# Optimization experiments

Measured on AMD Instinct MI355X. Metric: run time of the kernel, lower is better.

## Reference

```python
import jax, jax.numpy as jnp
import numpy as np

D_LATENTS = 256
B, N = 8, 4096
EPS = 1e-5  # BatchNorm eps (torch default)


def _w(k, shape):
    return jax.random.normal(k, shape, jnp.float32) * 0.05


def setup_inputs() -> dict:
    key = jax.random.key(0)
    ks = jax.random.split(key, 20)
    d4, d2, d = D_LATENTS // 4, D_LATENTS // 2, D_LATENTS
    def bn(k):
        k1, k2 = jax.random.split(k)
        g = 1.0 + 0.1 * jax.random.normal(k1, (0,), jnp.float32)  # placeholder
        return g
    inp = {
        "x": jax.random.normal(ks[0], (B, 3, N), jnp.float32),
        "conv1_w": _w(ks[1], (d4, 3)),
        "bn1_g": 1.0 + 0.1 * jax.random.normal(ks[2], (d4,), jnp.float32),
        "bn1_b": 0.1 * jax.random.normal(ks[3], (d4,), jnp.float32),
        "conv2_w": _w(ks[4], (d4, d4)),
        "bn2_g": 1.0 + 0.1 * jax.random.normal(ks[5], (d4,), jnp.float32),
        "bn2_b": 0.1 * jax.random.normal(ks[6], (d4,), jnp.float32),
        "le0_w1": _w(ks[7], (d2, d2)),
        "le0_g1": 1.0 + 0.1 * jax.random.normal(ks[8], (d2,), jnp.float32),
        "le0_b1": 0.1 * jax.random.normal(ks[9], (d2,), jnp.float32),
        "le0_w2": _w(ks[10], (d2, d2)),
        "le0_g2": 1.0 + 0.1 * jax.random.normal(ks[11], (d2,), jnp.float32),
        "le0_b2": 0.1 * jax.random.normal(ks[12], (d2,), jnp.float32),
        "le1_w1": _w(ks[13], (d, d)),
        "le1_g1": 1.0 + 0.1 * jax.random.normal(ks[14], (d,), jnp.float32),
        "le1_b1": 0.1 * jax.random.normal(ks[15], (d,), jnp.float32),
        "le1_w2": _w(ks[16], (d, d)),
        "le1_g2": 1.0 + 0.1 * jax.random.normal(ks[17], (d,), jnp.float32),
        "le1_b2": 0.1 * jax.random.normal(ks[18], (d,), jnp.float32),
    }
    return inp


def _bn_relu(y, g, b, axes, ch_axis):
    # BatchNorm (training-mode batch stats, biased var like torch) + ReLU
    m = jnp.mean(y, axes, keepdims=True)
    v = jnp.var(y, axes, keepdims=True)
    shp = [1] * y.ndim
    shp[ch_axis] = -1
    return jax.nn.relu((y - m) * jax.lax.rsqrt(v + EPS) * g.reshape(shp) + b.reshape(shp))


def _square_distance(src, dst):
    # src [B,S,3], dst [B,N,3] -> [B,S,N]
    return (jnp.sum(src * src, -1, keepdims=True)
            - 2.0 * jnp.einsum('bsc,bnc->bsn', src, dst)
            + jnp.sum(dst * dst, -1)[:, None, :])


def _fps(xyz, npoint):
    # farthest point sampling, deterministic start at index 0
    Bb, Nn, _ = xyz.shape
    def step(carry, _):
        dist_min, farthest = carry
        centroid = jnp.take_along_axis(xyz, farthest[:, None, None], axis=1)  # [B,1,3]
        d = jnp.sum((xyz - centroid) ** 2, -1)  # [B,N]
        dist_min = jnp.minimum(dist_min, d)
        nxt = jnp.argmax(dist_min, -1).astype(jnp.int32)
        return (dist_min, nxt), farthest
    init = (jnp.full((Bb, Nn), 1e10, xyz.dtype), jnp.zeros((Bb,), jnp.int32))
    _, idxs = jax.lax.scan(step, init, None, length=npoint)
    return jnp.transpose(idxs)  # [B, npoint]


def _sample_and_group(npoint, nsample, xyz, points):
    # PCT-style: FPS centers, kNN neighbors (radius unused), concat(rel, center)
    Bb = xyz.shape[0]
    fps_idx = _fps(xyz, npoint)                       # [B,S]
    bidx = jnp.arange(Bb)[:, None]
    new_xyz = xyz[bidx, fps_idx]                      # [B,S,3]
    new_pts = points[bidx, fps_idx]                   # [B,S,D]
    d2 = _square_distance(new_xyz, xyz)               # [B,S,N]
    _, knn_idx = jax.lax.top_k(-d2, nsample)          # [B,S,ns]
    grouped = points[jnp.arange(Bb)[:, None, None], knn_idx]  # [B,S,ns,D]
    center = new_pts[:, :, None, :]
    feat = jnp.concatenate([grouped - center,
                            jnp.broadcast_to(center, grouped.shape)], axis=-1)
    return new_xyz, feat  # [B,S,3], [B,S,ns,2D]


def _local_encoder(x4, w1, g1, b1, w2, g2, b2):
    # x4: [b,n,s,d] -> conv1x1/bn/relu x2 over channel dim, max over s -> [b,out,n]
    y = jnp.einsum('bnsd,od->bnos', x4, w1)
    y = _bn_relu(y, g1, b1, (0, 1, 3), 2)
    y = jnp.einsum('bnis,oi->bnos', y, w2)
    y = _bn_relu(y, g2, b2, (0, 1, 3), 2)
    y = jnp.max(y, axis=3)                # [b,n,out]
    return jnp.transpose(y, (0, 2, 1))    # [b,out,n]


def reference(x, conv1_w, bn1_g, bn1_b, conv2_w, bn2_g, bn2_b,
              le0_w1, le0_g1, le0_b1, le0_w2, le0_g2, le0_b2,
              le1_w1, le1_g1, le1_b1, le1_w2, le1_g2, le1_b2):
    xyz = jnp.transpose(x, (0, 2, 1))                 # [B,N,3]
    y = jnp.einsum('bcn,oc->bon', x, conv1_w)
    y = _bn_relu(y, bn1_g, bn1_b, (0, 2), 1)
    y = jnp.einsum('bcn,oc->bon', y, conv2_w)
    y = _bn_relu(y, bn2_g, bn2_b, (0, 2), 1)
    pts = jnp.transpose(y, (0, 2, 1))                 # [B,N,d4]
    new_xyz, feat = _sample_and_group(512, 32, xyz, pts)       # [B,512,32,d2]
    f0 = _local_encoder(feat, le0_w1, le0_g1, le0_b1, le0_w2, le0_g2, le0_b2)  # [B,d2,512]
    pts1 = jnp.transpose(f0, (0, 2, 1))
    _, feat2 = _sample_and_group(256, 32, new_xyz, pts1)       # [B,256,32,d]
    f1 = _local_encoder(feat2, le1_w1, le1_g1, le1_b1, le1_w2, le1_g2, le1_b2)  # [B,d,256]
    return f1
```

## Files before the change

### kernel.cpp

```cpp
#include <hip/hip_runtime.h>

constexpr int B_  = 8;
constexpr int N_  = 4096;
constexpr int NP1 = 512;
constexpr int NP2 = 256;
constexpr float EPS_ = 1e-5f;

typedef __attribute__((ext_vector_type(8))) short bhalf8;
typedef __attribute__((ext_vector_type(4))) float f32x4;

__device__ inline short f2bf(float f) {
  union { float fv; unsigned u; } v; v.fv = f;
  unsigned r = v.u + 0x7FFFu + ((v.u >> 16) & 1u);
  return (short)(r >> 16);
}

template<int CTRL>
__device__ inline void dpp_amax(unsigned &khi, unsigned &klo) {
  unsigned ohi = (unsigned)__builtin_amdgcn_mov_dpp((int)khi, CTRL, 0xF, 0xF, false);
  unsigned olo = (unsigned)__builtin_amdgcn_mov_dpp((int)klo, CTRL, 0xF, 0xF, false);
  if (ohi > khi || (ohi == khi && olo > klo)) { khi = ohi; klo = olo; }
}
__device__ inline void swz16_amax(unsigned &khi, unsigned &klo) {
  unsigned ohi = (unsigned)__builtin_amdgcn_ds_swizzle((int)khi, 0x401F);
  unsigned olo = (unsigned)__builtin_amdgcn_ds_swizzle((int)klo, 0x401F);
  if (ohi > khi || (ohi == khi && olo > klo)) { khi = ohi; klo = olo; }
}
__device__ inline void x32_amax(unsigned &khi, unsigned &klo) {
  unsigned ohi = (unsigned)__shfl_xor((int)khi, 32);
  unsigned olo = (unsigned)__shfl_xor((int)klo, 32);
  if (ohi > khi || (ohi == khi && olo > klo)) { khi = ohi; klo = olo; }
}
__device__ inline unsigned ford(float f) {
  unsigned u = __float_as_uint(f);
  return u ^ (((unsigned)((int)u >> 31)) | 0x80000000u);
}

constexpr int S_BN1 = 0;
constexpr int S_BN2 = 128;
constexpr int S_L0A = 256;
constexpr int S_L0B = 512;
constexpr int S_L1A = 768;
constexpr int S_L1B = 1280;
constexpr int S_TOTAL = 1792;

constexpr size_t OFF_T1   = 0;
constexpr size_t OFF_YBUF = OFF_T1   + 2097152;
constexpr size_t OFF_PTS1 = OFF_YBUF + 16777216;
constexpr size_t OFF_NXYZ = OFF_PTS1 + 524288;
constexpr size_t OFF_WT2C = OFF_NXYZ + 12288;
constexpr size_t OFF_BW0A = OFF_WT2C + 4096;
constexpr size_t OFF_BW0B = OFF_BW0A + 8192;
constexpr size_t OFF_BW1A = OFF_BW0B + 8192;
constexpr size_t OFF_BW1B = OFF_BW1A + 32768;
constexpr size_t OFF_STAT = OFF_BW1B + 32768;
constexpr size_t OFF_CNT  = OFF_STAT + S_TOTAL;
constexpr size_t OFF_INT  = OFF_CNT + 32;

__device__ inline void prep_elem(int idx, const float* __restrict__ conv2w,
                                 const float* __restrict__ w0a, const float* __restrict__ w0b,
                                 const float* __restrict__ w1a, const float* __restrict__ w1b,
                                 float* __restrict__ wt2c,
                                 short* __restrict__ b0a, short* __restrict__ b0b,
                                 short* __restrict__ b1a, short* __restrict__ b1b) {
  if (idx < 4096) { int d = idx >> 6, o = idx & 63; wt2c[idx] = conv2w[o*64 + d]; return; }
  idx -= 4096;
  const float* w; short* dst; int D;
  if      (idx <  2048) { w = w0a; dst = b0a; D = 128; }
  else if (idx <  4096) { w = w0b; dst = b0b; D = 128; idx -= 2048; }
  else if (idx < 12288) { w = w1a; dst = b1a; D = 256; idx -= 4096; }
  else                  { w = w1b; dst = b1b; D = 256; idx -= 12288; }
  int kblk = idx / D, o = idx % D;
  const float* src = w + (size_t)o*D + kblk*8;
  bhalf8 pk;
#pragma unroll
  for (int j = 0; j < 8; ++j) pk[j] = f2bf(src[j]);
  *(bhalf8*)&dst[(size_t)idx*8] = pk;
}

struct FpsSmem {
  float lx[4096], ly[4096], lz[4096];
  float sx[512], sy[512], sz[512];
  unsigned long long wk[2][8];
  int seli1[512];
  int seli2[256];
};
struct ConvSmem {
  float xs[3][64];
  float redS[4][64], redQ[4][64];
  float sc[64], sh[64];
  float at[64*68];
};

__global__ __launch_bounds__(256) void front_kernel(
    const float* __restrict__ x,
    const float* __restrict__ conv1w, const float* __restrict__ bn1g, const float* __restrict__ bn1b,
    const float* __restrict__ conv2w, const float* __restrict__ bn2g, const float* __restrict__ bn2b,
    const float* __restrict__ w0a, const float* __restrict__ w0b,
    const float* __restrict__ w1a, const float* __restrict__ w1b,
    float* __restrict__ wt2c,
    short* __restrict__ b0a, short* __restrict__ b0b,
    short* __restrict__ b1a, short* __restrict__ b1b,
    float* __restrict__ t1, float* __restrict__ t2,
    float* __restrict__ stats, int* __restrict__ cnt,
    int* __restrict__ sel1, float* __restrict__ nxyz, int* __restrict__ sel2) {
  __shared__ __align__(16) char smem_raw[sizeof(FpsSmem)];
  int t = threadIdx.x;
  if (blockIdx.x < 8) {
    constexpr int NPTS = 4096, NSEL1 = 512, NSEL2 = 256, NT = 256;
    constexpr int K = NPTS / NT, NS = NT / 32;
    FpsSmem& S = *reinterpret_cast<FpsSmem*>(smem_raw);
    int b = blockIdx.x;
    int lane = t & 63, wid = t >> 6;
    const float* cb = x + (size_t)b * 3 * NPTS;
    for (int i = t; i < NPTS; i += NT) {
      S.lx[i] = cb[i]; S.ly[i] = cb[NPTS + i]; S.lz[i] = cb[2*NPTS + i];
    }
    __syncthreads();
    float px[K], py[K], pz[K], dm[K];
#pragma unroll
    for (int k = 0; k < K; ++k) {
      int p = t + k*NT;
      px[k] = S.lx[p]; py[k] = S.ly[p]; pz[k] = S.lz[p];
      dm[k] = 1e10f;
    }
    float cx = S.lx[0], cy = S.ly[0], cz = S.lz[0];
    if (t == 0) { S.seli1[0] = 0; S.sx[0] = cx; S.sy[0] = cy; S.sz[0] = cz; }
    for (int it = 1; it < NSEL1; ++it) {
      float bv = -1.f; int bi = 0;
#pragma unroll
      for (int k = 0; k < K; ++k) {
        float dx = px[k]-cx, dy = py[k]-cy, dz = pz[k]-cz;
        float d = dx*dx + dy*dy + dz*dz;
        float nd = fminf(dm[k], d);
        dm[k] = nd;
        if (nd > bv) { bv = nd; bi = t + k*NT; }
      }
      unsigned khi = __float_as_uint(bv), klo = ~(unsigned)bi;
      dpp_amax<0xB1>(khi, klo);
      dpp_amax<0x4E>(khi, klo);
      dpp_amax<0x141>(khi, klo);
      dpp_amax<0x140>(khi, klo);
      swz16_amax(khi, klo);
      int p = it & 1;
      if ((lane & 31) == 0)
        S.wk[p][wid*2 + (lane >> 5)] = ((unsigned long long)khi << 32) | klo;
      __syncthreads();
      unsigned long long best = S.wk[p][0];
#pragma unroll
      for (int i2 = 1; i2 < NS; ++i2) { unsigned long long v2 = S.wk[p][i2]; if (v2 > best) best = v2; }
      int Bi = (int)(~(unsigned)best);
      cx = S.lx[Bi]; cy = S.ly[Bi]; cz = S.lz[Bi];
      if (t == 0) { S.seli1[it] = Bi; S.sx[it] = cx; S.sy[it] = cy; S.sz[it] = cz; }
    }
    __syncthreads();
    if (t < 64) {
      constexpr int K2 = NSEL1 / 64;
      float qx[K2], qy[K2], qz[K2], dm2[K2];
#pragma unroll
      for (int k = 0; k < K2; ++k) {
        int p = t + k*64;
        qx[k] = S.sx[p]; qy[k] = S.sy[p]; qz[k] = S.sz[p];
        dm2[k] = 1e10f;
      }
      cx = S.sx[0]; cy = S.sy[0]; cz = S.sz[0];
      if (t == 0) S.seli2[0] = 0;
      for (int it = 1; it < NSEL2; ++it) {
        float bv = -1.f; int bi = 0;
#pragma unroll
        for (int k = 0; k < K2; ++k) {
          float dx = qx[k]-cx, dy = qy[k]-cy, dz = qz[k]-cz;
          float d = dx*dx + dy*dy + dz*dz;
          float nd = fminf(dm2[k], d);
          dm2[k] = nd;
          if (nd > bv) { bv = nd; bi = t + k*64; }
        }
        unsigned khi = __float_as_uint(bv), klo = ~(unsigned)bi;
        dpp_amax<0xB1>(khi, klo);
        dpp_amax<0x4E>(khi, klo);
        dpp_amax<0x141>(khi, klo);
        dpp_amax<0x140>(khi, klo);
        swz16_amax(khi, klo);
        x32_amax(khi, klo);
        int Bi = (int)~klo;
        cx = S.sx[Bi]; cy = S.sy[Bi]; cz = S.sz[Bi];
        if (t == 0) S.seli2[it] = Bi;
      }
    } else {
      for (int i = t - 64; i < NSEL1; i += NT - 64) {
        sel1[(size_t)b*NSEL1 + i] = S.seli1[i];
        float* q = nxyz + ((size_t)b*NSEL1 + i)*3;
        q[0] = S.sx[i]; q[1] = S.sy[i]; q[2] = S.sz[i];
      }
    }
    __syncthreads();
    for (int i = t; i < NSEL2; i += NT) sel2[(size_t)b*NSEL2 + i] = S.seli2[i];
    return;
  }
  ConvSmem& C = *reinterpret_cast<ConvSmem*>(smem_raw);
  int cb = blockIdx.x - 8;
  { int idx = cb*256 + t;
    if (idx < 24576) prep_elem(idx, conv2w, w0a, w0b, w1a, w1b, wt2c, b0a, b0b, b1a, b1b); }
  for (int tile = cb; tile < 512; tile += 256) {
    int b = tile >> 6, n0 = (tile & 63) << 6;
    if (t < 192) { int c = t >> 6, nl = t & 63; C.xs[c][nl] = x[((size_t)b*3 + c)*N_ + n0 + nl]; }
    __syncthreads();
    int o = t & 63, ng = t >> 6;
    float w0 = conv1w[o*3+0], w1 = conv1w[o*3+1], w2 = conv1w[o*3+2];
    float ls = 0.f, lq = 0.f;
#pragma unroll
    for (int k = 0; k < 16; ++k) {
      int nl = ng*16 + k;
      float y = C.xs[0][nl]*w0 + C.xs[1][nl]*w1 + C.xs[2][nl]*w2;
      t1[((size_t)b*N_ + n0 + nl)*64 + o] = y;
      ls += y; lq += y*y;
    }
    C.redS[ng][o] = ls; C.redQ[ng][o] = lq;
    __syncthreads();
    if (t < 64) {
      float s = C.redS[0][t]+C.redS[1][t]+C.redS[2][t]+C.redS[3][t];
      float q = C.redQ[0][t]+C.redQ[1][t]+C.redQ[2][t]+C.redQ[3][t];
      atomicAdd(&stats[S_BN1 + t], s);
      atomicAdd(&stats[S_BN1 + 64 + t], q);
    }
    __syncthreads();
  }
  if (t == 0) {
    __threadfence();
    __hip_atomic_fetch_add(&cnt[0], 1, __ATOMIC_ACQ_REL, __HIP_MEMORY_SCOPE_AGENT);
    while (__hip_atomic_load(&cnt[0], __ATOMIC_ACQUIRE, __HIP_MEMORY_SCOPE_AGENT) < 256)
      __builtin_amdgcn_s_sleep(8);
    __threadfence();
  }
  __syncthreads();
  if (t < 64) {
    float m = stats[S_BN1 + t] * (1.f/32768.f);
    float v = stats[S_BN1 + 64 + t] * (1.f/32768.f) - m*m;
    float s = bn1g[t] * rsqrtf(v + EPS_);
    C.sc[t] = s; C.sh[t] = bn1b[t] - m*s;
  }
  __syncthreads();
  for (int tile = cb; tile < 512; tile += 256) {
    int b = tile >> 6, n0 = (tile & 63) << 6;
    constexpr int P = 68;
    for (int e = t; e < 4096; e += 256) {
      int nl = e >> 6, c = e & 63;
      float v = t1[((size_t)b*N_ + n0 + nl)*64 + c];
      C.at[c*P + nl] = fmaxf(v*C.sc[c] + C.sh[c], 0.f);
    }
    __syncthreads();
    int o = t & 63, ng = t >> 6;
    float acc[16];
#pragma unroll
    for (int k = 0; k < 16; ++k) acc[k] = 0.f;
    for (int i = 0; i < 64; ++i) {
      float wv = wt2c[i*64 + o];
      const float* ar = &C.at[i*P + ng*16];
#pragma unroll
      for (int k = 0; k < 16; k += 4) {
        float4 a4 = *(const float4*)(ar + k);
        acc[k+0] += a4.x*wv; acc[k+1] += a4.y*wv;
        acc[k+2] += a4.z*wv; acc[k+3] += a4.w*wv;
      }
    }
    float ls = 0.f, lq = 0.f;
#pragma unroll
    for (int k = 0; k < 16; ++k) {
      float y = acc[k];
      t2[((size_t)b*N_ + n0 + ng*16 + k)*64 + o] = y;
      ls += y; lq += y*y;
    }
    C.redS[ng][o] = ls; C.redQ[ng][o] = lq;
    __syncthreads();
    if (t < 64) {
      float s = C.redS[0][t]+C.redS[1][t]+C.redS[2][t]+C.redS[3][t];
      float q = C.redQ[0][t]+C.redQ[1][t]+C.redQ[2][t]+C.redQ[3][t];
      atomicAdd(&stats[S_BN2 + t], s);
      atomicAdd(&stats[S_BN2 + 64 + t], q);
    }
    __syncthreads();
  }
  if (t == 0) {
    __threadfence();
    __hip_atomic_fetch_add(&cnt[1], 1, __ATOMIC_ACQ_REL, __HIP_MEMORY_SCOPE_AGENT);
    while (__hip_atomic_load(&cnt[1], __ATOMIC_ACQUIRE, __HIP_MEMORY_SCOPE_AGENT) < 256)
      __builtin_amdgcn_s_sleep(8);
    __threadfence();
  }
  __syncthreads();
  {
    int o = t & 63;
    float m = stats[S_BN2 + o] * (1.f/32768.f);
    float v = stats[S_BN2 + 64 + o] * (1.f/32768.f) - m*m;
    float s = bn2g[o] * rsqrtf(v + EPS_);
    float sh = bn2b[o] - m*s;
    for (int tile = cb; tile < 512; tile += 256)
#pragma unroll
      for (int j = 0; j < 16; ++j) {
        size_t idx = (size_t)tile*4096 + j*256 + t;
        t1[idx] = fmaxf(t2[idx]*s + sh, 0.f);
      }
  }
}

template<int NDST, bool XLAY>
__device__ inline void wave_knn(const float* __restrict__ db,
                                float qx, float qy, float qz,
                                int* __restrict__ out32) {
  constexpr int K = NDST / 64;
  int lane = threadIdx.x & 63;
  float q2 = (qx*qx + qy*qy) + qz*qz;
  float d2r[K];
#pragma unroll
  for (int k = 0; k < K; ++k) {
    int j = lane + k*64;
    float xx, yy, zz;
    if (XLAY) { xx = db[j]; yy = db[NDST + j]; zz = db[2*NDST + j]; }
    else      { xx = db[j*3]; yy = db[j*3+1]; zz = db[j*3+2]; }
    float dot = (qx*xx + qy*yy) + qz*zz;
    float p2  = (xx*xx + yy*yy) + zz*zz;
    d2r[k] = (q2 - 2.f*dot) + p2;
  }
  int myout = 0;
  for (int r = 0; r < 32; ++r) {
    float bv = 3e38f; int bi = lane;
#pragma unroll
    for (int k = 0; k < K; ++k) {
      float v = d2r[k];
      if (v < bv) { bv = v; bi = lane + k*64; }
    }
    unsigned khi = ~ford(bv), klo = ~(unsigned)bi;
    dpp_amax<0xB1>(khi, klo);
    dpp_amax<0x4E>(khi, klo);
    dpp_amax<0x141>(khi, klo);
    dpp_amax<0x140>(khi, klo);
    swz16_amax(khi, klo);
    x32_amax(khi, klo);
    int Bi = (int)~klo;
    if (lane == r) myout = Bi;
#pragma unroll
    for (int k = 0; k < K; ++k)
      if (lane + k*64 == Bi) d2r[k] = 3e38f;
  }
  if (lane < 32) out32[lane] = myout;
}

__global__ __launch_bounds__(256) void knn_fused_kernel(
    const float* __restrict__ x, const float* __restrict__ nxyz,
    const int* __restrict__ sel2, int* __restrict__ knn1, int* __restrict__ knn2) {
  int wid = threadIdx.x >> 6;
  int blk = blockIdx.x;
  if (blk < 1024) {
    int q = blk*4 + wid;
    int b = q >> 9, qi = q & 511;
    const float* qp = nxyz + ((size_t)b*NP1 + qi)*3;
    wave_knn<4096, true>(x + (size_t)b*3*N_, qp[0], qp[1], qp[2], knn1 + (size_t)q*32);
  } else {
    int q = (blk - 1024)*4 + wid;
    int b = q >> 8, qi = q & 255;
    int qrow = b*NP1 + sel2[b*NP2 + qi];
    const float* qp = nxyz + (size_t)qrow*3;
    wave_knn<512, false>(nxyz + (size_t)b*NP1*3, qp[0], qp[1], qp[2], knn2 + (size_t)q*32);
  }
}

template<int D, int PW, int NP, int SRCN, int SOFF>
__global__ __launch_bounds__(256) void gemm1_kernel(
    const float* __restrict__ pts, const int* __restrict__ knn,
    const int* __restrict__ cent, const short* __restrict__ bw,
    float* __restrict__ ybuf, float* __restrict__ stats) {
  constexpr int KB = D/8;
  __shared__ __align__(16) short As[64*D];
  __shared__ float cen_s[2*PW];
  __shared__ int kid_s[64];
  __shared__ float sstat[2*D];
  int t = threadIdx.x, blk = blockIdx.x;
  int g0 = blk*2;
  if (t < 64) {
    int grp = t >> 5, s = t & 31;
    kid_s[t] = knn[((size_t)(g0+grp))*32 + s];
  }
  for (int i = t; i < 2*PW; i += 256) {
    int grp = i / PW, d = i % PW;
    int g = g0 + grp; int b = g / NP; int ci = cent[g];
    cen_s[i] = pts[((size_t)b*SRCN + ci)*PW + d];
  }
  for (int i = t; i < 2*D; i += 256) sstat[i] = 0.f;
  __syncthreads();
  for (int task = t; task < 64*KB; task += 256) {
    int row = task / KB, c = task % KB;
    int grp = row >> 5;
    int g = g0 + grp; int b = g / NP;
    int d = c*8;
    float v0,v1,v2,v3,v4,v5,v6,v7;
    if (d < PW) {
      const float* src = pts + ((size_t)b*SRCN + kid_s[row])*PW + d;
      float4 x0 = *(const float4*)src, x1 = *(const float4*)(src+4);
      const float* cc = &cen_s[grp*PW + d];
      v0=x0.x-cc[0]; v1=x0.y-cc[1]; v2=x0.z-cc[2]; v3=x0.w-cc[3];
      v4=x1.x-cc[4]; v5=x1.y-cc[5]; v6=x1.z-cc[6]; v7=x1.w-cc[7];
    } else {
      const float* cc = &cen_s[grp*PW + d - PW];
      v0=cc[0]; v1=cc[1]; v2=cc[2]; v3=cc[3]; v4=cc[4]; v5=cc[5]; v6=cc[6]; v7=cc[7];
    }
    bhalf8 pk;
    pk[0]=f2bf(v0); pk[1]=f2bf(v1); pk[2]=f2bf(v2); pk[3]=f2bf(v3);
    pk[4]=f2bf(v4); pk[5]=f2bf(v5); pk[6]=f2bf(v6); pk[7]=f2bf(v7);
    int a16 = row*KB + (c ^ (row & 7));
    *(bhalf8*)&As[a16*8] = pk;
  }
  __syncthreads();
  int w = t >> 6, l = t & 63, lr = l & 15, lg = l >> 4;
  f32x4 acc[D/16];
#pragma unroll
  for (int ct = 0; ct < D/16; ++ct) acc[ct] = (f32x4){0.f,0.f,0.f,0.f};
  int r = w*16 + lr;
#pragma unroll
  for (int kg = 0; kg < D/32; ++kg) {
    int c = (kg*4 + lg) ^ (r & 7);
    bhalf8 af = *(const bhalf8*)&As[(r*KB + c)*8];
#pragma unroll
    for (int ct = 0; ct < D/16; ++ct) {
      bhalf8 bf = *(const bhalf8*)&bw[((size_t)(kg*4 + lg)*D + ct*16 + lr)*8];
      acc[ct] = __builtin_amdgcn_mfma_f32_16x16x32_bf16(af, bf, acc[ct], 0, 0, 0);
    }
  }
  size_t rb = (size_t)blk*64 + w*16 + lg*4;
#pragma unroll
  for (int ct = 0; ct < D/16; ++ct) {
    int col = ct*16 + lr;
    f32x4 a = acc[ct];
    float* yp = ybuf + rb*D + col;
    yp[0] = a[0]; yp[(size_t)D] = a[1]; yp[(size_t)2*D] = a[2]; yp[(size_t)3*D] = a[3];
    float s = a[0]+a[1]+a[2]+a[3];
    float q = a[0]*a[0]+a[1]*a[1]+a[2]*a[2]+a[3]*a[3];
    s += __shfl_xor(s, 16); q += __shfl_xor(q, 16);
    s += __shfl_xor(s, 32); q += __shfl_xor(q, 32);
    if (lg == 0) { atomicAdd(&sstat[col], s); atomicAdd(&sstat[D+col], q); }
  }
  __syncthreads();
  for (int i = t; i < 2*D; i += 256) atomicAdd(&stats[SOFF+i], sstat[i]);
}

template<int D, int SIN, int SOUT, int CNT>
__global__ __launch_bounds__(256) void gemm2_kernel(
    const float* __restrict__ g1, const float* __restrict__ b1,
    const short* __restrict__ bw, const float* __restrict__ ybuf,
    float* __restrict__ mm, float* __restrict__ stats) {
  __shared__ __align__(16) float scsh[2*D];
  __shared__ float sstat[2*D];
  __shared__ float wmax[4][D], wmin[4][D];
  int t = threadIdx.x, blk = blockIdx.x;
  for (int i = t; i < D; i += 256) {
    float m = stats[SIN + i] * (1.f/(float)CNT);
    float v = stats[SIN + D + i] * (1.f/(float)CNT) - m*m;
    float s = g1[i] * rsqrtf(v + EPS_);
    scsh[i] = s; scsh[D+i] = b1[i] - m*s;
  }
  for (int i = t; i < 2*D; i += 256) sstat[i] = 0.f;
  __syncthreads();
  int w = t >> 6, l = t & 63, lr = l & 15, lg = l >> 4;
  size_t row = (size_t)blk*64 + w*16 + lr;
  const float* yrow = ybuf + row*D;
  f32x4 acc[D/16];
#pragma unroll
  for (int ct = 0; ct < D/16; ++ct) acc[ct] = (f32x4){0.f,0.f,0.f,0.f};
#pragma unroll
  for (int kg = 0; kg < D/32; ++kg) {
    int k = kg*32 + lg*8;
    float4 y0 = *(const float4*)(yrow + k);
    float4 y1 = *(const float4*)(yrow + k + 4);
    bhalf8 af;
    af[0] = f2bf(fmaxf(y0.x*scsh[k+0] + scsh[D+k+0], 0.f));
    af[1] = f2bf(fmaxf(y0.y*scsh[k+1] + scsh[D+k+1], 0.f));
    af[2] = f2bf(fmaxf(y0.z*scsh[k+2] + scsh[D+k+2], 0.f));
    af[3] = f2bf(fmaxf(y0.w*scsh[k+3] + scsh[D+k+3], 0.f));
    af[4] = f2bf(fmaxf(y1.x*scsh[k+4] + scsh[D+k+4], 0.f));
    af[5] = f2bf(fmaxf(y1.y*scsh[k+5] + scsh[D+k+5], 0.f));
    af[6] = f2bf(fmaxf(y1.z*scsh[k+6] + scsh[D+k+6], 0.f));
    af[7] = f2bf(fmaxf(y1.w*scsh[k+7] + scsh[D+k+7], 0.f));
#pragma unroll
    for (int ct = 0; ct < D/16; ++ct) {
      bhalf8 bf = *(const bhalf8*)&bw[((size_t)(kg*4 + lg)*D + ct*16 + lr)*8];
      acc[ct] = __builtin_amdgcn_mfma_f32_16x16x32_bf16(af, bf, acc[ct], 0, 0, 0);
    }
  }
#pragma unroll
  for (int ct = 0; ct < D/16; ++ct) {
    int col = ct*16 + lr;
    f32x4 a = acc[ct];
    float mx = fmaxf(fmaxf(a[0], a[1]), fmaxf(a[2], a[3]));
    float mn = fminf(fminf(a[0], a[1]), fminf(a[2], a[3]));
    mx = fmaxf(mx, __shfl_xor(mx, 16)); mn = fminf(mn, __shfl_xor(mn, 16));
    mx = fmaxf(mx, __shfl_xor(mx, 32)); mn = fminf(mn, __shfl_xor(mn, 32));
    if (lg == 0) { wmax[w][col] = mx; wmin[w][col] = mn; }
    float s = a[0]+a[1]+a[2]+a[3];
    float q = a[0]*a[0]+a[1]*a[1]+a[2]*a[2]+a[3]*a[3];
    s += __shfl_xor(s, 16); q += __shfl_xor(q, 16);
    s += __shfl_xor(s, 32); q += __shfl_xor(q, 32);
    if (lg == 0) { atomicAdd(&sstat[col], s); atomicAdd(&sstat[D+col], q); }
  }
  __syncthreads();
  for (int i = t; i < 2*D; i += 256) {
    int g = i / D, col = i - g*D;
    float mx = fmaxf(wmax[2*g][col], wmax[2*g+1][col]);
    float mn = fminf(wmin[2*g][col], wmin[2*g+1][col]);
    float* mp = mm + ((size_t)blk*2 + g)*2*D;
    mp[col] = mx; mp[D + col] = mn;
    atomicAdd(&stats[SOUT+i], sstat[i]);
  }
}

template<int D, int NP, int SOFF, int CNT, bool TR>
__global__ __launch_bounds__(256) void le3_kernel(
    const float* __restrict__ g2, const float* __restrict__ b2,
    const float* __restrict__ mm, const float* __restrict__ stats,
    float* __restrict__ out) {
  int idx = blockIdx.x*256 + threadIdx.x;
  int g = idx / D, o = idx - g*D;
  float m = stats[SOFF + o] * (1.f/(float)CNT);
  float v = stats[SOFF + D + o] * (1.f/(float)CNT) - m*m;
  float s = g2[o] * rsqrtf(v + EPS_);
  float sh = b2[o] - m*s;
  const float* mp = mm + (size_t)g*2*D;
  float pick = (s >= 0.f) ? mp[o] : mp[D + o];
  float r = fmaxf(pick*s + sh, 0.f);
  if (TR) { int b = g / NP, n = g - b*NP; out[((size_t)b*D + o)*NP + n] = r; }
  else    out[(size_t)g*D + o] = r;
}

extern "C" void kernel_launch(void* const* d_in, const int* in_sizes, int n_in,
                              void* d_out, int out_size, void* d_ws, size_t ws_size,
                              hipStream_t stream) {
  (void)in_sizes; (void)n_in; (void)out_size; (void)ws_size;
  const float* x       = (const float*)d_in[0];
  const float* conv1_w = (const float*)d_in[1];
  const float* bn1_g   = (const float*)d_in[2];
  const float* bn1_b   = (const float*)d_in[3];
  const float* conv2_w = (const float*)d_in[4];
  const float* bn2_g   = (const float*)d_in[5];
  const float* bn2_b   = (const float*)d_in[6];
  const float* le0_w1  = (const float*)d_in[7];
  const float* le0_g1  = (const float*)d_in[8];
  const float* le0_b1  = (const float*)d_in[9];
  const float* le0_w2  = (const float*)d_in[10];
  const float* le0_g2  = (const float*)d_in[11];
  const float* le0_b2  = (const float*)d_in[12];
  const float* le1_w1  = (const float*)d_in[13];
  const float* le1_g1  = (const float*)d_in[14];
  const float* le1_b1  = (const float*)d_in[15];
  const float* le1_w2  = (const float*)d_in[16];
  const float* le1_g2  = (const float*)d_in[17];
  const float* le1_b2  = (const float*)d_in[18];

  float* ws   = (float*)d_ws;
  float* t1   = ws + OFF_T1;
  float* ybuf = ws + OFF_YBUF;
  float* t2   = ybuf;
  float* mm   = t1;
  float* pts1 = ws + OFF_PTS1;
  float* nxyz = ws + OFF_NXYZ;
  float* wt2c = ws + OFF_WT2C;
  short* bw0a = (short*)(ws + OFF_BW0A);
  short* bw0b = (short*)(ws + OFF_BW0B);
  short* bw1a = (short*)(ws + OFF_BW1A);
  short* bw1b = (short*)(ws + OFF_BW1B);
  float* stats = ws + OFF_STAT;
  int*   cnt   = (int*)(ws + OFF_CNT);
  int* fps1 = (int*)(ws + OFF_INT);
  int* fps2 = fps1 + 4096;
  int* knn1 = fps2 + 2048;
  int* knn2 = knn1 + 131072;

  hipMemsetAsync(stats, 0, (S_TOTAL + 32)*sizeof(float), stream);
  front_kernel<<<264, 256, 0, stream>>>(x,
      conv1_w, bn1_g, bn1_b, conv2_w, bn2_g, bn2_b,
      le0_w1, le0_w2, le1_w1, le1_w2,
      wt2c, bw0a, bw0b, bw1a, bw1b,
      t1, t2, stats, cnt, fps1, nxyz, fps2);

  knn_fused_kernel<<<1536, 256, 0, stream>>>(x, nxyz, fps2, knn1, knn2);

  gemm1_kernel<128,  64, 512, 4096, S_L0A><<<2048, 256, 0, stream>>>(t1, knn1, fps1, bw0a, ybuf, stats);
  gemm2_kernel<128, S_L0A, S_L0B, 131072><<<2048, 256, 0, stream>>>(le0_g1, le0_b1, bw0b, ybuf, mm, stats);
  le3_kernel<128, 512, S_L0B, 131072, false><<<2048, 256, 0, stream>>>(le0_g2, le0_b2, mm, stats, pts1);

  gemm1_kernel<256, 128, 256,  512, S_L1A><<<1024, 256, 0, stream>>>(pts1, knn2, fps2, bw1a, ybuf, stats);
  gemm2_kernel<256, S_L1A, S_L1B, 65536><<<1024, 256, 0, stream>>>(le1_g1, le1_b1, bw1b, ybuf, mm, stats);
  le3_kernel<256, 256, S_L1B, 65536, true><<<2048, 256, 0, stream>>>(le1_g2, le1_b2, mm, stats, (float*)d_out);
}
```

Measured before the change: 926.7 us.

## Overlap FPS with kNN and first grouped GEMM via in-kernel flags

The FPS blocks now publish selected centroids in chunks of 64 and raise per-batch/chunk flags. The remaining persistent blocks of the front kernel spin on those flags, run kNN for ready queries, then run the first local-encoder GEMM once all 64 kNN results of a chunk are done, and finally compute the second-level kNN after the sel2 flag. This removes two kernel launches and hides kNN and GEMM1 behind the serial FPS loop. In exchange it relies on co-residency of all 264 blocks for spin-waits, adds sync overhead and atomics, and serializes GEMM1 onto 248 blocks instead of 2048.

Measured after the change: 1.532 ms. 65.3% more time.

```diff
diff --git a/kernel.cpp b/kernel.cpp
--- a/kernel.cpp
+++ b/kernel.cpp
@@ -34,6 +34,26 @@
 __device__ inline unsigned ford(float f) {
   unsigned u = __float_as_uint(f);
   return u ^ (((unsigned)((int)u >> 31)) | 0x80000000u);
+}
+
+__device__ inline void set_flag_after_sync(int* f) {
+  if (threadIdx.x == 0) {
+    __threadfence();
+    __hip_atomic_store(f, 1, __ATOMIC_RELEASE, __HIP_MEMORY_SCOPE_AGENT);
+  }
+}
+__device__ inline void wave_wait_flag(int* f) {
+  while (__hip_atomic_load(f, __ATOMIC_ACQUIRE, __HIP_MEMORY_SCOPE_AGENT) == 0)
+    __builtin_amdgcn_s_sleep(32);
+  __threadfence();
+}
+__device__ inline void block_wait_count(int* f, int target) {
+  if (threadIdx.x == 0) {
+    while (__hip_atomic_load(f, __ATOMIC_ACQUIRE, __HIP_MEMORY_SCOPE_AGENT) < target)
+      __builtin_amdgcn_s_sleep(16);
+    __threadfence();
+  }
+  __syncthreads();
 }
 
 constexpr int S_BN1 = 0;
@@ -43,6 +63,11 @@
 constexpr int S_L1A = 768;
 constexpr int S_L1B = 1280;
 constexpr int S_TOTAL = 1792;
+
+constexpr int F_CHUNK = 8;
+constexpr int F_SEL2  = 72;
+constexpr int F_K1D   = 80;
+constexpr int CNT_N   = 160;
 
 constexpr size_t OFF_T1   = 0;
 constexpr size_t OFF_YBUF = OFF_T1   + 2097152;
@@ -55,7 +80,7 @@
 constexpr size_t OFF_BW1B = OFF_BW1A + 32768;
 constexpr size_t OFF_STAT = OFF_BW1B + 32768;
 constexpr size_t OFF_CNT  = OFF_STAT + S_TOTAL;
-constexpr size_t OFF_INT  = OFF_CNT + 32;
+constexpr size_t OFF_INT  = OFF_CNT + CNT_N;
 
 __device__ inline void prep_elem(int idx, const float* __restrict__ conv2w,
                                  const float* __restrict__ w0a, const float* __restrict__ w0b,
@@ -92,6 +117,126 @@
   float at[64*68];
 };
 
+template<int NDST, bool XLAY>
+__device__ inline void wave_knn(const float* __restrict__ db,
+                                float qx, float qy, float qz,
+                                int* __restrict__ out32) {
+  constexpr int K = NDST / 64;
+  int lane = threadIdx.x & 63;
+  float q2 = (qx*qx + qy*qy) + qz*qz;
+  float d2r[K];
+#pragma unroll
+  for (int k = 0; k < K; ++k) {
+    int j = lane + k*64;
+    float xx, yy, zz;
+    if (XLAY) { xx = db[j]; yy = db[NDST + j]; zz = db[2*NDST + j]; }
+    else      { xx = db[j*3]; yy = db[j*3+1]; zz = db[j*3+2]; }
+    float dot = (qx*xx + qy*yy) + qz*zz;
+    float p2  = (xx*xx + yy*yy) + zz*zz;
+    d2r[k] = (q2 - 2.f*dot) + p2;
+  }
+  int myout = 0;
+  for (int r = 0; r < 32; ++r) {
+    float bv = 3e38f; int bi = lane;
+#pragma unroll
+    for (int k = 0; k < K; ++k) {
+      float v = d2r[k];
+      if (v < bv) { bv = v; bi = lane + k*64; }
+    }
+    unsigned khi = ~ford(bv), klo = ~(unsigned)bi;
+    dpp_amax<0xB1>(khi, klo);
+    dpp_amax<0x4E>(khi, klo);
+    dpp_amax<0x141>(khi, klo);
+    dpp_amax<0x140>(khi, klo);
+    swz16_amax(khi, klo);
+    x32_amax(khi, klo);
+    int Bi = (int)~klo;
+    if (lane == r) myout = Bi;
+#pragma unroll
+    for (int k = 0; k < K; ++k)
+      if (lane + k*64 == Bi) d2r[k] = 3e38f;
+  }
+  if (lane < 32) out32[lane] = myout;
+}
+
+template<int D, int PW, int NP, int SRCN, int SOFF>
+__device__ void gemm1_body(int blk, const float* __restrict__ pts, const int* __restrict__ knn,
+                           const int* __restrict__ cent, const short* __restrict__ bw,
+                           float* __restrict__ ybuf, float* __restrict__ stats, char* smem) {
+  constexpr int KB = D/8;
+  short* As     = (short*)smem;
+  float* cen_s  = (float*)(smem + 64*D*2);
+  int*   kid_s  = (int*)(smem + 64*D*2 + 2*PW*4);
+  float* sstat  = (float*)(smem + 64*D*2 + 2*PW*4 + 256);
+  int t = threadIdx.x;
+  int g0 = blk*2;
+  if (t < 64) {
+    int grp = t >> 5, s = t & 31;
+    kid_s[t] = knn[((size_t)(g0+grp))*32 + s];
+  }
+  for (int i = t; i < 2*PW; i += 256) {
+    int grp = i / PW, d = i % PW;
+    int g = g0 + grp; int b = g / NP; int ci = cent[g];
+    cen_s[i] = pts[((size_t)b*SRCN + ci)*PW + d];
+  }
+  for (int i = t; i < 2*D; i += 256) sstat[i] = 0.f;
+  __syncthreads();
+  for (int task = t; task < 64*KB; task += 256) {
+    int row = task / KB, c = task % KB;
+    int grp = row >> 5;
+    int g = g0 + grp; int b = g / NP;
+    int d = c*8;
+    float v0,v1,v2,v3,v4,v5,v6,v7;
+    if (d < PW) {
+      const float* src = pts + ((size_t)b*SRCN + kid_s[row])*PW + d;
+      float4 x0 = *(const float4*)src, x1 = *(const float4*)(src+4);
+      const float* cc = &cen_s[grp*PW + d];
+      v0=x0.x-cc[0]; v1=x0.y-cc[1]; v2=x0.z-cc[2]; v3=x0.w-cc[3];
+      v4=x1.x-cc[4]; v5=x1.y-cc[5]; v6=x1.z-cc[6]; v7=x1.w-cc[7];
+    } else {
+      const float* cc = &cen_s[grp*PW + d - PW];
+      v0=cc[0]; v1=cc[1]; v2=cc[2]; v3=cc[3]; v4=cc[4]; v5=cc[5]; v6=cc[6]; v7=cc[7];
+    }
+    bhalf8 pk;
+    pk[0]=f2bf(v0); pk[1]=f2bf(v1); pk[2]=f2bf(v2); pk[3]=f2bf(v3);
+    pk[4]=f2bf(v4); pk[5]=f2bf(v5); pk[6]=f2bf(v6); pk[7]=f2bf(v7);
+    int a16 = row*KB + (c ^ (row & 7));
+    *(bhalf8*)&As[a16*8] = pk;
+  }
+  __syncthreads();
+  int w = t >> 6, l = t & 63, lr = l & 15, lg = l >> 4;
+  f32x4 acc[D/16];
+#pragma unroll
+  for (int ct = 0; ct < D/16; ++ct) acc[ct] = (f32x4){0.f,0.f,0.f,0.f};
+  int r = w*16 + lr;
+#pragma unroll
+  for (int kg = 0; kg < D/32; ++kg) {
+    int c = (kg*4 + lg) ^ (r & 7);
+    bhalf8 af = *(const bhalf8*)&As[(r*KB + c)*8];
+#pragma unroll
+    for (int ct = 0; ct < D/16; ++ct) {
+      bhalf8 bf = *(const bhalf8*)&bw[((size_t)(kg*4 + lg)*D + ct*16 + lr)*8];
+      acc[ct] = __builtin_amdgcn_mfma_f32_16x16x32_bf16(af, bf, acc[ct], 0, 0, 0);
+    }
+  }
+  size_t rb = (size_t)blk*64 + w*16 + lg*4;
+#pragma unroll
+  for (int ct = 0; ct < D/16; ++ct) {
+    int col = ct*16 + lr;
+    f32x4 a = acc[ct];
+    float* yp = ybuf + rb*D + col;
+    yp[0] = a[0]; yp[(size_t)D] = a[1]; yp[(size_t)2*D] = a[2]; yp[(size_t)3*D] = a[3];
+    float s = a[0]+a[1]+a[2]+a[3];
+    float q = a[0]*a[0]+a[1]*a[1]+a[2]*a[2]+a[3]*a[3];
+    s += __shfl_xor(s, 16); q += __shfl_xor(q, 16);
+    s += __shfl_xor(s, 32); q += __shfl_xor(q, 32);
+    if (lg == 0) { atomicAdd(&sstat[col], s); atomicAdd(&sstat[D+col], q); }
+  }
+  __syncthreads();
+  for (int i = t; i < 2*D; i += 256) atomicAdd(&stats[SOFF+i], sstat[i]);
+  __syncthreads();
+}
+
 __global__ __launch_bounds__(256) void front_kernel(
     const float* __restrict__ x,
     const float* __restrict__ conv1w, const float* __restrict__ bn1g, const float* __restrict__ bn1b,
@@ -103,7 +248,9 @@
     short* __restrict__ b1a, short* __restrict__ b1b,
     float* __restrict__ t1, float* __restrict__ t2,
     float* __restrict__ stats, int* __restrict__ cnt,
-    int* __restrict__ sel1, float* __restrict__ nxyz, int* __restrict__ sel2) {
+    int* __restrict__ sel1, float* __restrict__ nxyz, int* __restrict__ sel2,
+    int* __restrict__ knn1, int* __restrict__ knn2,
+    float* __restrict__ ybuf) {
   __shared__ __align__(16) char smem_raw[sizeof(FpsSmem)];
   int t = threadIdx.x;
   if (blockIdx.x < 8) {
@@ -152,6 +299,18 @@
       int Bi = (int)(~(unsigned)best);
       cx = S.lx[Bi]; cy = S.ly[Bi]; cz = S.lz[Bi];
       if (t == 0) { S.seli1[it] = Bi; S.sx[it] = cx; S.sy[it] = cy; S.sz[it] = cz; }
+      if ((it & 63) == 63) {
+        __syncthreads();
+        int c = it >> 6;
+        if (t < 64) {
+          int i = c*64 + t;
+          sel1[(size_t)b*NSEL1 + i] = S.seli1[i];
+          float* q = nxyz + ((size_t)b*NSEL1 + i)*3;
+          q[0] = S.sx[i]; q[1] = S.sy[i]; q[2] = S.sz[i];
+        }
+        __syncthreads();
+        set_flag_after_sync(&cnt[F_CHUNK + b*8 + c]);
+      }
     }
     __syncthreads();
     if (t < 64) {
@@ -186,181 +345,174 @@
         cx = S.sx[Bi]; cy = S.sy[Bi]; cz = S.sz[Bi];
         if (t == 0) S.seli2[it] = Bi;
       }
-    } else {
-      for (int i = t - 64; i < NSEL1; i += NT - 64) {
-        sel1[(size_t)b*NSEL1 + i] = S.seli1[i];
-        float* q = nxyz + ((size_t)b*NSEL1 + i)*3;
-        q[0] = S.sx[i]; q[1] = S.sy[i]; q[2] = S.sz[i];
-      }
     }
     __syncthreads();
     for (int i = t; i < NSEL2; i += NT) sel2[(size_t)b*NSEL2 + i] = S.seli2[i];
+    __syncthreads();
+    set_flag_after_sync(&cnt[F_SEL2 + b]);
     return;
   }
-  ConvSmem& C = *reinterpret_cast<ConvSmem*>(smem_raw);
-  int cb = blockIdx.x - 8;
-  { int idx = cb*256 + t;
-    if (idx < 24576) prep_elem(idx, conv2w, w0a, w0b, w1a, w1b, wt2c, b0a, b0b, b1a, b1b); }
-  for (int tile = cb; tile < 512; tile += 256) {
-    int b = tile >> 6, n0 = (tile & 63) << 6;
-    if (t < 192) { int c = t >> 6, nl = t & 63; C.xs[c][nl] = x[((size_t)b*3 + c)*N_ + n0 + nl]; }
-    __syncthreads();
-    int o = t & 63, ng = t >> 6;
-    float w0 = conv1w[o*3+0], w1 = conv1w[o*3+1], w2 = conv1w[o*3+2];
-    float ls = 0.f, lq = 0.f;
-#pragma unroll
-    for (int k = 0; k < 16; ++k) {
-      int nl = ng*16 + k;
-      float y = C.xs[0][nl]*w0 + C.xs[1][nl]*w1 + C.xs[2][nl]*w2;
-      t1[((size_t)b*N_ + n0 + nl)*64 + o] = y;
-      ls += y; lq += y*y;
-    }
-    C.redS[ng][o] = ls; C.redQ[ng][o] = lq;
+  {
+    ConvSmem& C = *reinterpret_cast<ConvSmem*>(smem_raw);
+    int cb = blockIdx.x - 8;
+    { int idx = cb*256 + t;
+      if (idx < 24576) prep_elem(idx, conv2w, w0a, w0b, w1a, w1b, wt2c, b0a, b0b, b1a, b1b); }
+    for (int tile = cb; tile < 512; tile += 256) {
+      int b = tile >> 6, n0 = (tile & 63) << 6;
+      if (t < 192) { int c = t >> 6, nl = t & 63; C.xs[c][nl] = x[((size_t)b*3 + c)*N_ + n0 + nl]; }
+      __syncthreads();
+      int o = t & 63, ng = t >> 6;
+      float w0 = conv1w[o*3+0], w1 = conv1w[o*3+1], w2 = conv1w[o*3+2];
+      float ls = 0.f, lq = 0.f;
+#pragma unroll
+      for (int k = 0; k < 16; ++k) {
+        int nl = ng*16 + k;
+        float y = C.xs[0][nl]*w0 + C.xs[1][nl]*w1 + C.xs[2][nl]*w2;
+        t1[((size_t)b*N_ + n0 + nl)*64 + o] = y;
+        ls += y; lq += y*y;
+      }
+      C.redS[ng][o] = ls; C.redQ[ng][o] = lq;
+      __syncthreads();
+      if (t < 64) {
+        float s = C.redS[0][t]+C.redS[1][t]+C.redS[2][t]+C.redS[3][t];
+        float q = C.redQ[0][t]+C.redQ[1][t]+C.redQ[2][t]+C.redQ[3][t];
+        atomicAdd(&stats[S_BN1 + t], s);
+        atomicAdd(&stats[S_BN1 + 64 + t], q);
+      }
+      __syncthreads();
+    }
+    if (t == 0) {
+      __threadfence();
+      __hip_atomic_fetch_add(&cnt[0], 1, __ATOMIC_ACQ_REL, __HIP_MEMORY_SCOPE_AGENT);
+      while (__hip_atomic_load(&cnt[0], __ATOMIC_ACQUIRE, __HIP_MEMORY_SCOPE_AGENT) < 256)
+        __builtin_amdgcn_s_sleep(8);
+      __threadfence();
+    }
     __syncthreads();
     if (t < 64) {
-      float s = C.redS[0][t]+C.redS[1][t]+C.redS[2][t]+C.redS[3][t];
-      float q = C.redQ[0][t]+C.redQ[1][t]+C.redQ[2][t]+C.redQ[3][t];
-      atomicAdd(&stats[S_BN1 + t], s);
-      atomicAdd(&stats[S_BN1 + 64 + t], q);
-    }
-    __syncthreads();
-  }
-  if (t == 0) {
-    __threadfence();
-    __hip_atomic_fetch_add(&cnt[0], 1, __ATOMIC_ACQ_REL, __HIP_MEMORY_SCOPE_AGENT);
-    while (__hip_atomic_load(&cnt[0], __ATOMIC_ACQUIRE, __HIP_MEMORY_SCOPE_AGENT) < 256)
-      __builtin_amdgcn_s_sleep(8);
-    __threadfence();
-  }
-  __syncthreads();
-  if (t < 64) {
-    float m = stats[S_BN1 + t] * (1.f/32768.f);
-    float v = stats[S_BN1 + 64 + t] * (1.f/32768.f) - m*m;
-    float s = bn1g[t] * rsqrtf(v + EPS_);
-    C.sc[t] = s; C.sh[t] = bn1b[t] - m*s;
-  }
-  __syncthreads();
-  for (int tile = cb; tile < 512; tile += 256) {
-    int b = tile >> 6, n0 = (tile & 63) << 6;
-    constexpr int P = 68;
-    for (int e = t; e < 4096; e += 256) {
-      int nl = e >> 6, c = e & 63;
-      float v = t1[((size_t)b*N_ + n0 + nl)*64 + c];
-      C.at[c*P + nl] = fmaxf(v*C.sc[c] + C.sh[c], 0.f);
-    }
-    __syncthreads();
-    int o = t & 63, ng = t >> 6;
-    float acc[16];
-#pragma unroll
-    for (int k = 0; k < 16; ++k) acc[k] = 0.f;
-    for (int i = 0; i < 64; ++i) {
-      float wv = wt2c[i*64 + o];
-      const float* ar = &C.at[i*P + ng*16];
-#pragma unroll
-      for (int k = 0; k < 16; k += 4) {
-        float4 a4 = *(const float4*)(ar + k);
-        acc[k+0] += a4.x*wv; acc[k+1] += a4.y*wv;
-        acc[k+2] += a4.z*wv; acc[k+3] += a4.w*wv;
-      }
-    }
-    float ls = 0.f, lq = 0.f;
-#pragma unroll
-    for (int k = 0; k < 16; ++k) {
-      float y = acc[k];
-      t2[((size_t)b*N_ + n0 + ng*16 + k)*64 + o] = y;
-      ls += y; lq += y*y;
-    }
-    C.redS[ng][o] = ls; C.redQ[ng][o] = lq;
-    __syncthreads();
-    if (t < 64) {
-      float s = C.redS[0][t]+C.redS[1][t]+C.redS[2][t]+C.redS[3][t];
-      float q = C.redQ[0][t]+C.redQ[1][t]+C.redQ[2][t]+C.redQ[3][t];
-      atomicAdd(&stats[S_BN2 + t], s);
-      atomicAdd(&stats[S_BN2 + 64 + t], q);
-    }
-    __syncthreads();
-  }
-  if (t == 0) {
-    __threadfence();
-    __hip_atomic_fetch_add(&cnt[1], 1, __ATOMIC_ACQ_REL, __HIP_MEMORY_SCOPE_AGENT);
-    while (__hip_atomic_load(&cnt[1], __ATOMIC_ACQUIRE, __HIP_MEMORY_SCOPE_AGENT) < 256)
-      __builtin_amdgcn_s_sleep(8);
-    __threadfence();
-  }
-  __syncthreads();
+      float m = stats[S_BN1 + t] * (1.f/32768.f);
+      float v = stats[S_BN1 + 64 + t] * (1.f/32768.f) - m*m;
+      float s = bn1g[t] * rsqrtf(v + EPS_);
+      C.sc[t] = s; C.sh[t] = bn1b[t] - m*s;
+    }
+    __syncthreads();
+    for (int tile = cb; tile < 512; tile += 256) {
+      int b = tile >> 6, n0 = (tile & 63) << 6;
+      constexpr int P = 68;
+      for (int e = t; e < 4096; e += 256) {
+        int nl = e >> 6, c = e & 63;
+        float v = t1[((size_t)b*N_ + n0 + nl)*64 + c];
+        C.at[c*P + nl] = fmaxf(v*C.sc[c] + C.sh[c], 0.f);
+      }
+      __syncthreads();
+      int o = t & 63, ng = t >> 6;
+      float acc[16];
+#pragma unroll
+      for (int k = 0; k < 16; ++k) acc[k] = 0.f;
+      for (int i = 0; i < 64; ++i) {
+        float wv = wt2c[i*64 + o];
+        const float* ar = &C.at[i*P + ng*16];
+#pragma unroll
+        for (int k = 0; k < 16; k += 4) {
+          float4 a4 = *(const float4*)(ar + k);
+          acc[k+0] += a4.x*wv; acc[k+1] += a4.y*wv;
+          acc[k+2] += a4.z*wv; acc[k+3] += a4.w*wv;
+        }
+      }
+      float ls = 0.f, lq = 0.f;
+#pragma unroll
+      for (int k = 0; k < 16; ++k) {
+        float y = acc[k];
+        t2[((size_t)b*N_ + n0 + ng*16 + k)*64 + o] = y;
+        ls += y; lq += y*y;
+      }
+      C.redS[ng][o] = ls; C.redQ[ng][o] = lq;
+      __syncthreads();
+      if (t < 64) {
+        float s = C.redS[0][t]+C.redS[1][t]+C.redS[2][t]+C.redS[3][t];
+        float q = C.redQ[0][t]+C.redQ[1][t]+C.redQ[2][t]+C.redQ[3][t];
+        atomicAdd(&stats[S_BN2 + t], s);
+        atomicAdd(&stats[S_BN2 + 64 + t], q);
+      }
+      __syncthreads();
+    }
+    if (t == 0) {
+      __threadfence();
+      __hip_atomic_fetch_add(&cnt[1], 1, __ATOMIC_ACQ_REL, __HIP_MEMORY_SCOPE_AGENT);
+      while (__hip_atomic_load(&cnt[1], __ATOMIC_ACQUIRE, __HIP_MEMORY_SCOPE_AGENT) < 256)
+        __builtin_amdgcn_s_sleep(8);
+      __threadfence();
+    }
+    __syncthreads();
+    {
+      int o = t & 63;
+      float m = stats[S_BN2 + o] * (1.f/32768.f);
+      float v = stats[S_BN2 + 64 + o] * (1.f/32768.f) - m*m;
+      float s = bn2g[o] * rsqrtf(v + EPS_);
+      float sh = bn2b[o] - m*s;
+      for (int tile = cb; tile < 512; tile += 256)
+#pragma unroll
+        for (int j = 0; j < 16; ++j) {
+          size_t idx = (size_t)tile*4096 + j*256 + t;
+          t1[idx] = fmaxf(t2[idx]*s + sh, 0.f);
+        }
+    }
+    __syncthreads();
+    if (t == 0) {
+      __threadfence();
+      __hip_atomic_fetch_add(&cnt[2], 1, __ATOMIC_ACQ_REL, __HIP_MEMORY_SCOPE_AGENT);
+      while (__hip_atomic_load(&cnt[2], __ATOMIC_ACQUIRE, __HIP_MEMORY_SCOPE_AGENT) < 256)
+        __builtin_amdgcn_s_sleep(8);
+      __threadfence();
+    }
+    __syncthreads();
+    if (cb >= 248) return;
+  }
   {
-    int o = t & 63;
-    float m = stats[S_BN2 + o] * (1.f/32768.f);
-    float v = stats[S_BN2 + 64 + o] * (1.f/32768.f) - m*m;
-    float s = bn2g[o] * rsqrtf(v + EPS_);
-    float sh = bn2b[o] - m*s;
-    for (int tile = cb; tile < 512; tile += 256)
-#pragma unroll
-      for (int j = 0; j < 16; ++j) {
-        size_t idx = (size_t)tile*4096 + j*256 + t;
-        t1[idx] = fmaxf(t2[idx]*s + sh, 0.f);
-      }
-  }
-}
-
-template<int NDST, bool XLAY>
-__device__ inline void wave_knn(const float* __restrict__ db,
-                                float qx, float qy, float qz,
-                                int* __restrict__ out32) {
-  constexpr int K = NDST / 64;
-  int lane = threadIdx.x & 63;
-  float q2 = (qx*qx + qy*qy) + qz*qz;
-  float d2r[K];
-#pragma unroll
-  for (int k = 0; k < K; ++k) {
-    int j = lane + k*64;
-    float xx, yy, zz;
-    if (XLAY) { xx = db[j]; yy = db[NDST + j]; zz = db[2*NDST + j]; }
-    else      { xx = db[j*3]; yy = db[j*3+1]; zz = db[j*3+2]; }
-    float dot = (qx*xx + qy*yy) + qz*zz;
-    float p2  = (xx*xx + yy*yy) + zz*zz;
-    d2r[k] = (q2 - 2.f*dot) + p2;
-  }
-  int myout = 0;
-  for (int r = 0; r < 32; ++r) {
-    float bv = 3e38f; int bi = lane;
-#pragma unroll
-    for (int k = 0; k < K; ++k) {
-      float v = d2r[k];
-      if (v < bv) { bv = v; bi = lane + k*64; }
-    }
-    unsigned khi = ~ford(bv), klo = ~(unsigned)bi;
-    dpp_amax<0xB1>(khi, klo);
-    dpp_amax<0x4E>(khi, klo);
-    dpp_amax<0x141>(khi, klo);
-    dpp_amax<0x140>(khi, klo);
-    swz16_amax(khi, klo);
-    x32_amax(khi, klo);
-    int Bi = (int)~klo;
-    if (lane == r) myout = Bi;
-#pragma unroll
-    for (int k = 0; k < K; ++k)
-      if (lane + k*64 == Bi) d2r[k] = 3e38f;
-  }
-  if (lane < 32) out32[lane] = myout;
-}
-
-__global__ __launch_bounds__(256) void knn_fused_kernel(
-    const float* __restrict__ x, const float* __restrict__ nxyz,
-    const int* __restrict__ sel2, int* __restrict__ knn1, int* __restrict__ knn2) {
-  int wid = threadIdx.x >> 6;
-  int blk = blockIdx.x;
-  if (blk < 1024) {
-    int q = blk*4 + wid;
-    int b = q >> 9, qi = q & 511;
-    const float* qp = nxyz + ((size_t)b*NP1 + qi)*3;
-    wave_knn<4096, true>(x + (size_t)b*3*N_, qp[0], qp[1], qp[2], knn1 + (size_t)q*32);
-  } else {
-    int q = (blk - 1024)*4 + wid;
-    int b = q >> 8, qi = q & 255;
-    int qrow = b*NP1 + sel2[b*NP2 + qi];
-    const float* qp = nxyz + (size_t)qrow*3;
-    wave_knn<512, false>(nxyz + (size_t)b*NP1*3, qp[0], qp[1], qp[2], knn2 + (size_t)q*32);
+    int cb = blockIdx.x - 8;
+    int lane = t & 63;
+    int gw = cb*4 + (t >> 6);
+    int qi_i = 0, un_i = 0;
+    for (int c = 0; c <= 8; ++c) {
+      if (c < 8) {
+        while (true) {
+          int q_ord = gw + 992*qi_i;
+          if (q_ord >= 4096 || (q_ord >> 9) != c) break;
+          int bq = q_ord & 511; int b = bq >> 6; int qi = c*64 + (bq & 63);
+          wave_wait_flag(&cnt[F_CHUNK + b*8 + c]);
+          const float* qp = nxyz + ((size_t)b*NP1 + qi)*3;
+          wave_knn<4096, true>(x + (size_t)b*3*N_, qp[0], qp[1], qp[2],
+                               knn1 + ((size_t)b*NP1 + qi)*32);
+          __threadfence();
+          if (lane == 0)
+            __hip_atomic_fetch_add(&cnt[F_K1D + b*8 + c], 1, __ATOMIC_RELEASE, __HIP_MEMORY_SCOPE_AGENT);
+          ++qi_i;
+        }
+      }
+      __syncthreads();
+      if (c >= 1) {
+        while (true) {
+          int u_ord = cb + 248*un_i;
+          if (u_ord >= 2048 || (u_ord >> 8) != c-1) break;
+          int r = u_ord & 255; int b = r >> 5, p = r & 31;
+          int u = b*256 + 32*(c-1) + p;
+          block_wait_count(&cnt[F_K1D + b*8 + (c-1)], 64);
+          gemm1_body<128, 64, 512, 4096, S_L0A>(u, t1, knn1, sel1, b0a, ybuf, stats, smem_raw);
+          ++un_i;
+        }
+      }
+      __syncthreads();
+    }
+    for (int i2 = 0;; ++i2) {
+      int q = gw + 992*i2;
+      if (q >= 2048) break;
+      int b = q >> 8, qq = q & 255;
+      wave_wait_flag(&cnt[F_SEL2 + b]);
+      int qrow = b*NP1 + sel2[b*NP2 + qq];
+      const float* qp = nxyz + (size_t)qrow*3;
+      wave_knn<512, false>(nxyz + (size_t)b*NP1*3, qp[0], qp[1], qp[2],
+                           knn2 + (size_t)q*32);
+    }
   }
 }
 
@@ -369,77 +521,8 @@
     const float* __restrict__ pts, const int* __restrict__ knn,
     const int* __restrict__ cent, const short* __restrict__ bw,
     float* __restrict__ ybuf, float* __restrict__ stats) {
-  constexpr int KB = D/8;
-  __shared__ __align__(16) short As[64*D];
-  __shared__ float cen_s[2*PW];
-  __shared__ int kid_s[64];
-  __shared__ float sstat[2*D];
-  int t = threadIdx.x, blk = blockIdx.x;
-  int g0 = blk*2;
-  if (t < 64) {
-    int grp = t >> 5, s = t & 31;
-    kid_s[t] = knn[((size_t)(g0+grp))*32 + s];
-  }
-  for (int i = t; i < 2*PW; i += 256) {
-    int grp = i / PW, d = i % PW;
-    int g = g0 + grp; int b = g / NP; int ci = cent[g];
-    cen_s[i] = pts[((size_t)b*SRCN + ci)*PW + d];
-  }
-  for (int i = t; i < 2*D; i += 256) sstat[i] = 0.f;
-  __syncthreads();
-  for (int task = t; task < 64*KB; task += 256) {
-    int row = task / KB, c = task % KB;
-    int grp = row >> 5;
-    int g = g0 + grp; int b = g / NP;
-    int d = c*8;
-    float v0,v1,v2,v3,v4,v5,v6,v7;
-    if (d < PW) {
-      const float* src = pts + ((size_t)b*SRCN + kid_s[row])*PW + d;
-      float4 x0 = *(const float4*)src, x1 = *(const float4*)(src+4);
-      const float* cc = &cen_s[grp*PW + d];
-      v0=x0.x-cc[0]; v1=x0.y-cc[1]; v2=x0.z-cc[2]; v3=x0.w-cc[3];
-      v4=x1.x-cc[4]; v5=x1.y-cc[5]; v6=x1.z-cc[6]; v7=x1.w-cc[7];
-    } else {
-      const float* cc = &cen_s[grp*PW + d - PW];
-      v0=cc[0]; v1=cc[1]; v2=cc[2]; v3=cc[3]; v4=cc[4]; v5=cc[5]; v6=cc[6]; v7=cc[7];
-    }
-    bhalf8 pk;
-    pk[0]=f2bf(v0); pk[1]=f2bf(v1); pk[2]=f2bf(v2); pk[3]=f2bf(v3);
-    pk[4]=f2bf(v4); pk[5]=f2bf(v5); pk[6]=f2bf(v6); pk[7]=f2bf(v7);
-    int a16 = row*KB + (c ^ (row & 7));
-    *(bhalf8*)&As[a16*8] = pk;
-  }
-  __syncthreads();
-  int w = t >> 6, l = t & 63, lr = l & 15, lg = l >> 4;
-  f32x4 acc[D/16];
-#pragma unroll
-  for (int ct = 0; ct < D/16; ++ct) acc[ct] = (f32x4){0.f,0.f,0.f,0.f};
-  int r = w*16 + lr;
-#pragma unroll
-  for (int kg = 0; kg < D/32; ++kg) {
-    int c = (kg*4 + lg) ^ (r & 7);
-    bhalf8 af = *(const bhalf8*)&As[(r*KB + c)*8];
-#pragma unroll
-    for (int ct = 0; ct < D/16; ++ct) {
-      bhalf8 bf = *(const bhalf8*)&bw[((size_t)(kg*4 + lg)*D + ct*16 + lr)*8];
-      acc[ct] = __builtin_amdgcn_mfma_f32_16x16x32_bf16(af, bf, acc[ct], 0, 0, 0);
-    }
-  }
-  size_t rb = (size_t)blk*64 + w*16 + lg*4;
-#pragma unroll
-  for (int ct = 0; ct < D/16; ++ct) {
-    int col = ct*16 + lr;
-    f32x4 a = acc[ct];
-    float* yp = ybuf + rb*D + col;
-    yp[0] = a[0]; yp[(size_t)D] = a[1]; yp[(size_t)2*D] = a[2]; yp[(size_t)3*D] = a[3];
-    float s = a[0]+a[1]+a[2]+a[3];
-    float q = a[0]*a[0]+a[1]*a[1]+a[2]*a[2]+a[3]*a[3];
-    s += __shfl_xor(s, 16); q += __shfl_xor(q, 16);
-    s += __shfl_xor(s, 32); q += __shfl_xor(q, 32);
-    if (lg == 0) { atomicAdd(&sstat[col], s); atomicAdd(&sstat[D+col], q); }
-  }
-  __syncthreads();
-  for (int i = t; i < 2*D; i += 256) atomicAdd(&stats[SOFF+i], sstat[i]);
+  __shared__ __align__(16) char smem[64*D*2 + 2*PW*4 + 256 + 2*D*4];
+  gemm1_body<D, PW, NP, SRCN, SOFF>(blockIdx.x, pts, knn, cent, bw, ybuf, stats, smem);
 }
 
 template<int D, int SIN, int SOUT, int CNT>
@@ -572,16 +655,13 @@
   int* knn1 = fps2 + 2048;
   int* knn2 = knn1 + 131072;
 
-  hipMemsetAsync(stats, 0, (S_TOTAL + 32)*sizeof(float), stream);
+  hipMemsetAsync(stats, 0, (S_TOTAL + CNT_N)*sizeof(float), stream);
   front_kernel<<<264, 256, 0, stream>>>(x,
       conv1_w, bn1_g, bn1_b, conv2_w, bn2_g, bn2_b,
       le0_w1, le0_w2, le1_w1, le1_w2,
       wt2c, bw0a, bw0b, bw1a, bw1b,
-      t1, t2, stats, cnt, fps1, nxyz, fps2);
-
-  knn_fused_kernel<<<1536, 256, 0, stream>>>(x, nxyz, fps2, knn1, knn2);
-
-  gemm1_kernel<128,  64, 512, 4096, S_L0A><<<2048, 256, 0, stream>>>(t1, knn1, fps1, bw0a, ybuf, stats);
+      t1, t2, stats, cnt, fps1, nxyz, fps2, knn1, knn2, ybuf);
+
   gemm2_kernel<128, S_L0A, S_L0B, 131072><<<2048, 256, 0, stream>>>(le0_g1, le0_b1, bw0b, ybuf, mm, stats);
   le3_kernel<128, 512, S_L0B, 131072, false><<<2048, 256, 0, stream>>>(le0_g2, le0_b2, mm, stats, pts1);
 
```
